# Kernel tuning notes

Hardware: AMD Instinct MI355X
Metric: run time of the kernel (lower is better)

## Reference

```python
import jax, jax.numpy as jnp
import numpy as np

DX, DZ, DT = 10.0, 10.0, 1.0e-3
NX, NZ = 512, 512
NSTEPS, NREC = 512, 128
DT2 = DT * DT
INV_DXDZ = 1.0 / (DX * DZ)


def setup_inputs() -> dict:
    key = jax.random.key(0)
    k1, k2, k3, k4 = jax.random.split(key, 4)
    # velocity in [1500, 2500] m/s -> CFL stable with dt=1e-3, dx=dz=10
    velocity_model = 1500.0 + 1000.0 * jax.random.uniform(k1, (NX, NZ), dtype=jnp.float32)
    source = jax.random.normal(k2, (NSTEPS,), dtype=jnp.float32)
    rec_x = jax.random.randint(k3, (NREC,), 0, NX)
    rec_z = jax.random.randint(k4, (NREC,), 0, NZ)
    return {
        "velocity_model": velocity_model,
        "source": source,
        "src_x": 256,
        "src_z": 8,
        "rec_x": rec_x,
        "rec_z": rec_z,
    }


def _laplacian(p):
    # 3x3 cross stencil with zero padding, scaled by 1/(dx*dz) -- identical to
    # F.conv2d(p, [[0,1,0],[1,-4,1],[0,1,0]]/(dx*dz), padding=1)
    pp = jnp.pad(p, 1)
    return (pp[:-2, 1:-1] + pp[2:, 1:-1] + pp[1:-1, :-2] + pp[1:-1, 2:] - 4.0 * p) * INV_DXDZ


def reference(velocity_model, source, src_x, src_z, rec_x, rec_z):
    v2_dt2 = velocity_model * velocity_model * DT2  # [nx, nz]

    def step(carry, s_t):
        p, p_old = carry
        p_new = 2.0 * p - p_old + v2_dt2 * _laplacian(p)
        p_new = p_new.at[src_x, src_z].add(s_t * DT2)
        return (p_new, p), p_new[rec_x, rec_z]  # gather all receivers at once

    p0 = jnp.zeros((NX, NZ), dtype=velocity_model.dtype)
    _, recs = jax.lax.scan(step, (p0, p0), source)  # recs: [n_steps, n_rec]
    return recs.T  # seismogram: [n_rec, n_steps]
```

## Files before the change

### kernel.cpp

```cpp
#include <hip/hip_runtime.h>


#define NXd 512
#define NZd 512
#define NSTEPSd 512
#define NRECd 128
#define DT2f 1.0e-6f
#define INVf 1.0e-2f
#define TBk 16
#define TIk 32
#define EXTk 64
#define NTILEk 16

__global__ __launch_bounds__(1024) void fdtd_tblock(
    const float* __restrict__ vel,
    const float* __restrict__ source,
    const int* __restrict__ src_x, const int* __restrict__ src_z,
    const int* __restrict__ rec_x, const int* __restrict__ rec_z,
    const float* __restrict__ Gc_in, const float* __restrict__ Go_in,
    float* __restrict__ Gc_out, float* __restrict__ Go_out,
    float* __restrict__ out, int t0)
{
    __shared__ float sb[2][EXTk * EXTk];

    const int tid = threadIdx.x;
    const int r0 = tid >> 6;
    const int ez = tid & 63;
    const int gx0 = blockIdx.y * TIk, gz0 = blockIdx.x * TIk;
    const int ox = gx0 - TBk, oz = gz0 - TBk;

    const int sx = *src_x, sz = *src_z;

    bool rOwn = false; int rIdx = 0;
    if (tid < NRECd) {
        int rx = rec_x[tid], rz = rec_z[tid];
        rOwn = (rx >= gx0 && rx < gx0 + TIk && rz >= gz0 && rz < gz0 + TIk);
        rIdx = (rx - gx0 + TBk) * EXTk + (rz - gz0 + TBk);
    }

    {
        int dxm = max(0, max(ox - sx, sx - (ox + EXTk - 1)));
        int dzm = max(0, max(oz - sz, sz - (oz + EXTk - 1)));
        if (dxm + dzm > t0 + TBk + 1) {
            if (rOwn) {
                #pragma unroll
                for (int s = 0; s < TBk; ++s)
                    out[tid * NSTEPSd + t0 + s] = 0.0f;
            }
            return;
        }
    }

    const int gz = oz + ez;
    const bool zin = (gz >= 0 && gz < NZd);
    float rCur[4], rOld[4], rV2[4];
    #pragma unroll
    for (int i = 0; i < 4; ++i) {
        const int ex = r0 + 16 * i;
        const int gx = ox + ex;
        float c = 0.0f, o = 0.0f, v2 = 0.0f;
        if (zin && gx >= 0 && gx < NXd) {
            const int g = gx * NZd + gz;
            c = Gc_in[g];
            o = Go_in[g];
            const float v = vel[g];
            v2 = v * v * DT2f;
        }
        rCur[i] = c; rOld[i] = o; rV2[i] = v2;
        sb[0][ex * EXTk + ez] = c;
        sb[1][ex * EXTk + ez] = c;
    }

    const int exs = sx - ox, ezs = sz - oz;
    const bool srcHere = (exs >= 0 && exs < EXTk && ezs >= 0 && ezs < EXTk) &&
                         (tid == (((exs & 15) << 6) | ezs));
    float sv[TBk];
    if (srcHere) {
        #pragma unroll
        for (int s = 0; s < TBk; ++s) sv[s] = source[t0 + s] * DT2f;
    }

    __syncthreads();

    #pragma unroll
    for (int s = 0; s < TBk; ++s) {
        const float* cur = sb[s & 1];
        float* nxt = sb[(s & 1) ^ 1];
        const int m = s + 1;
        const bool zv = (ez >= m) && (ez < EXTk - m);
        #pragma unroll
        for (int i = 0; i < 4; ++i) {
            const int ex = r0 + 16 * i;
            if (zv && ex >= m && ex < EXTk - m) {
                const float up = cur[(ex - 1) * EXTk + ez];
                const float dn = cur[(ex + 1) * EXTk + ez];
                const float lf = cur[ex * EXTk + ez - 1];
                const float rt = cur[ex * EXTk + ez + 1];
                const float lap = (up + dn + lf + rt - 4.0f * rCur[i]) * INVf;
                const float nv = 2.0f * rCur[i] - rOld[i] + rV2[i] * lap;
                rOld[i] = rCur[i];
                rCur[i] = nv;
                nxt[ex * EXTk + ez] = nv;
            }
        }
        if (srcHere && exs >= m && exs < EXTk - m && ezs >= m && ezs < EXTk - m) {
            #pragma unroll
            for (int i = 0; i < 4; ++i) {
                if (i == (exs >> 4)) {
                    rCur[i] += sv[s];
                    nxt[exs * EXTk + ezs] = rCur[i];
                }
            }
        }
        __syncthreads();
        if (rOwn) out[tid * NSTEPSd + t0 + s] = nxt[rIdx];
    }

    if (ez >= TBk && ez < EXTk - TBk) {
        #pragma unroll
        for (int i = 1; i <= 2; ++i) {
            const int ex = r0 + 16 * i;
            const int g = (ox + ex) * NZd + gz;
            Gc_out[g] = rCur[i];
            Go_out[g] = rOld[i];
        }
    }
}

extern "C" void kernel_launch(void* const* d_in, const int* in_sizes, int n_in,
                              void* d_out, int out_size, void* d_ws, size_t ws_size,
                              hipStream_t stream) {
    const float* vel    = (const float*)d_in[0];
    const float* source = (const float*)d_in[1];
    const int*   src_x  = (const int*)d_in[2];
    const int*   src_z  = (const int*)d_in[3];
    const int*   rec_x  = (const int*)d_in[4];
    const int*   rec_z  = (const int*)d_in[5];
    float* out = (float*)d_out;

    const size_t F = (size_t)NXd * NZd;
    float* A_c = (float*)d_ws;
    float* A_o = A_c + F;
    float* B_c = A_o + F;
    float* B_o = B_c + F;

    hipMemsetAsync(d_ws, 0, 4 * F * sizeof(float), stream);

    dim3 grid(NTILEk, NTILEk), block(1024);
    for (int k = 0; k < NSTEPSd / TBk; ++k) {
        const float *ic, *io; float *oc, *oo;
        if (k & 1) { ic = B_c; io = B_o; oc = A_c; oo = A_o; }
        else       { ic = A_c; io = A_o; oc = B_c; oo = B_o; }
        fdtd_tblock<<<grid, block, 0, stream>>>(vel, source, src_x, src_z,
                                                rec_x, rec_z, ic, io, oc, oo,
                                                out, k * TBk);
    }
}
```

Measured before the change: 415.0 us.

## Give each thread four consecutive rows and take horizontal neighbours via DPP lane shifts

Each thread now owns four consecutive rows of a column instead of four rows strided by 16. Vertical stencil neighbours therefore come from registers, with only one shared-memory read above and one below the group. Horizontal neighbours come from 64-lane DPP wave shifts instead of shared-memory loads, and the 1/(dx*dz) scale is folded into the per-point v²dt² coefficient. Per-step validity masks are dropped, so the outer halo computes garbage that never reaches the stored interior. This cuts LDS traffic and branching per step, at the cost of relying on wave-shift DPP semantics and on the halo width being large enough.

Result: faster. 374.1 us (-9.9%).

```diff
diff --git a/kernel.cpp b/kernel.cpp
--- a/kernel.cpp
+++ b/kernel.cpp
@@ -12,6 +12,17 @@
 #define EXTk 64
 #define NTILEk 16
 
+__device__ __forceinline__ float dpp_shr1(float x) {
+    int v = __builtin_amdgcn_update_dpp(0, __builtin_bit_cast(int, x),
+                                        0x138, 0xF, 0xF, false);
+    return __builtin_bit_cast(float, v);
+}
+__device__ __forceinline__ float dpp_shl1(float x) {
+    int v = __builtin_amdgcn_update_dpp(0, __builtin_bit_cast(int, x),
+                                        0x130, 0xF, 0xF, false);
+    return __builtin_bit_cast(float, v);
+}
+
 __global__ __launch_bounds__(1024) void fdtd_tblock(
     const float* __restrict__ vel,
     const float* __restrict__ source,
@@ -24,8 +35,8 @@
     __shared__ float sb[2][EXTk * EXTk];
 
     const int tid = threadIdx.x;
-    const int r0 = tid >> 6;
-    const int ez = tid & 63;
+    const int w   = tid >> 6;
+    const int ez  = tid & 63;
     const int gx0 = blockIdx.y * TIk, gz0 = blockIdx.x * TIk;
     const int ox = gx0 - TBk, oz = gz0 - TBk;
 
@@ -53,10 +64,10 @@
 
     const int gz = oz + ez;
     const bool zin = (gz >= 0 && gz < NZd);
-    float rCur[4], rOld[4], rV2[4];
+    float rCur[4], rOld[4], rV2i[4];
     #pragma unroll
     for (int i = 0; i < 4; ++i) {
-        const int ex = r0 + 16 * i;
+        const int ex = 4 * w + i;
         const int gx = ox + ex;
         float c = 0.0f, o = 0.0f, v2 = 0.0f;
         if (zin && gx >= 0 && gx < NXd) {
@@ -64,16 +75,17 @@
             c = Gc_in[g];
             o = Go_in[g];
             const float v = vel[g];
-            v2 = v * v * DT2f;
+            v2 = v * v * (DT2f * INVf);
         }
-        rCur[i] = c; rOld[i] = o; rV2[i] = v2;
+        rCur[i] = c; rOld[i] = o; rV2i[i] = v2;
         sb[0][ex * EXTk + ez] = c;
-        sb[1][ex * EXTk + ez] = c;
     }
+    const int rowUp = (w == 0)  ? 0             : 4 * w - 1;
+    const int rowDn = (w == 15) ? EXTk - 1      : 4 * w + 4;
 
     const int exs = sx - ox, ezs = sz - oz;
     const bool srcHere = (exs >= 0 && exs < EXTk && ezs >= 0 && ezs < EXTk) &&
-                         (tid == (((exs & 15) << 6) | ezs));
+                         (tid == (((exs >> 2) << 6) | ezs));
     float sv[TBk];
     if (srcHere) {
         #pragma unroll
@@ -86,27 +98,30 @@
     for (int s = 0; s < TBk; ++s) {
         const float* cur = sb[s & 1];
         float* nxt = sb[(s & 1) ^ 1];
-        const int m = s + 1;
-        const bool zv = (ez >= m) && (ez < EXTk - m);
+        const float up0 = cur[rowUp * EXTk + ez];
+        const float dn3 = cur[rowDn * EXTk + ez];
+        float nv[4];
         #pragma unroll
         for (int i = 0; i < 4; ++i) {
-            const int ex = r0 + 16 * i;
-            if (zv && ex >= m && ex < EXTk - m) {
-                const float up = cur[(ex - 1) * EXTk + ez];
-                const float dn = cur[(ex + 1) * EXTk + ez];
-                const float lf = cur[ex * EXTk + ez - 1];
-                const float rt = cur[ex * EXTk + ez + 1];
-                const float lap = (up + dn + lf + rt - 4.0f * rCur[i]) * INVf;
-                const float nv = 2.0f * rCur[i] - rOld[i] + rV2[i] * lap;
-                rOld[i] = rCur[i];
-                rCur[i] = nv;
-                nxt[ex * EXTk + ez] = nv;
-            }
+            const float up = (i == 0) ? up0 : rCur[i - 1];
+            const float dn = (i == 3) ? dn3 : rCur[i + 1];
+            const float lf = dpp_shr1(rCur[i]);
+            const float rt = dpp_shl1(rCur[i]);
+            const float sum = (up + dn) + (lf + rt);
+            const float t4 = __builtin_fmaf(-4.0f, rCur[i], sum);
+            const float pm = __builtin_fmaf(2.0f, rCur[i], -rOld[i]);
+            nv[i] = __builtin_fmaf(rV2i[i], t4, pm);
         }
-        if (srcHere && exs >= m && exs < EXTk - m && ezs >= m && ezs < EXTk - m) {
+        #pragma unroll
+        for (int i = 0; i < 4; ++i) {
+            rOld[i] = rCur[i];
+            rCur[i] = nv[i];
+            nxt[(4 * w + i) * EXTk + ez] = nv[i];
+        }
+        if (srcHere) {
             #pragma unroll
             for (int i = 0; i < 4; ++i) {
-                if (i == (exs >> 4)) {
+                if (i == (exs & 3)) {
                     rCur[i] += sv[s];
                     nxt[exs * EXTk + ezs] = rCur[i];
                 }
@@ -116,11 +131,10 @@
         if (rOwn) out[tid * NSTEPSd + t0 + s] = nxt[rIdx];
     }
 
-    if (ez >= TBk && ez < EXTk - TBk) {
+    if (w >= 4 && w < 12 && ez >= TBk && ez < EXTk - TBk) {
         #pragma unroll
-        for (int i = 1; i <= 2; ++i) {
-            const int ex = r0 + 16 * i;
-            const int g = (ox + ex) * NZd + gz;
+        for (int i = 0; i < 4; ++i) {
+            const int g = (ox + 4 * w + i) * NZd + gz;
             Gc_out[g] = rCur[i];
             Go_out[g] = rOld[i];
         }
```
